# Kernel tuning notes

Measured on AMD Instinct MI355X. Metric: run time of the kernel, lower is better.

Reference implementation:

```python
import jax, jax.numpy as jnp
import numpy as np

HIDDEN = 2048
INPUT = 128
BATCH = 2048


def setup_inputs() -> dict:
    key = jax.random.key(0)
    k = jax.random.split(key, 7)
    inp = {
        "input": jax.random.normal(k[0], (BATCH, INPUT), dtype=jnp.float32),
        "hx_real": jax.random.normal(k[1], (BATCH, HIDDEN), dtype=jnp.float32),
        "hx_imag": jax.random.normal(k[2], (BATCH, HIDDEN), dtype=jnp.float32),
        "W_unitary": jax.random.normal(k[3], (5 * HIDDEN, INPUT), dtype=jnp.float32) / np.sqrt(INPUT),
        "b_unitary": jax.random.normal(k[4], (5 * HIDDEN,), dtype=jnp.float32) * 0.01,
        "beta": jnp.zeros((HIDDEN,), dtype=jnp.float32),
        "permutation": jax.random.permutation(k[5], HIDDEN).astype(jnp.int32),
    }
    return inp


def _householder_apply(v, h):
    # (I - 2 v v^H) h = h - 2 v (v^H h); same math as materializing the matrix.
    proj = jnp.sum(jnp.conj(v) * h, axis=-1, keepdims=True)
    return h - 2.0 * v * proj


def reference(input, hx_real, hx_imag, W_unitary, b_unitary, beta, permutation):
    hx = hx_real + 1j * hx_imag  # (B, H) complex64
    up = input @ W_unitary.T + b_unitary  # (B, 5H)
    phases = jnp.exp(1j * up)  # complex64, unit modulus
    d1, d2, d3, r1, r2 = jnp.split(phases, 5, axis=-1)

    h = jnp.fft.fft(d1 * hx, axis=-1)
    h = _householder_apply(r1, h)
    h = jnp.fft.ifft(d2 * h[:, permutation], axis=-1)
    h = d3 * _householder_apply(r2, h)

    # ModReLU: relu(|z| + beta) * exp(1j * angle(z))
    mag = jnp.abs(h)
    new_mag = jax.nn.relu(mag + beta)
    h = new_mag * jnp.exp(1j * jnp.angle(h))
    return h
```

## Files before the change

kernel.cpp:

```cpp
#include <hip/hip_runtime.h>

#define HID 2048
#define FIVEH 10240
#define INP 128
#define BATCH 2048

typedef _Float16 half8 __attribute__((ext_vector_type(8)));
typedef float f32x4 __attribute__((ext_vector_type(4)));

__global__ __launch_bounds__(256) void convert_f16(const float* __restrict__ src,
                                                   _Float16* __restrict__ dst) {
  int idx = (blockIdx.x * 256 + threadIdx.x) * 8;
  float4 a = *(const float4*)(src + idx);
  float4 b = *(const float4*)(src + idx + 4);
  half8 h;
  h[0] = (_Float16)a.x; h[1] = (_Float16)a.y; h[2] = (_Float16)a.z; h[3] = (_Float16)a.w;
  h[4] = (_Float16)b.x; h[5] = (_Float16)b.y; h[6] = (_Float16)b.z; h[7] = (_Float16)b.w;
  *(half8*)(dst + idx) = h;
}

__global__ __launch_bounds__(256) void gemm_up(const _Float16* __restrict__ Ah,
                                               const _Float16* __restrict__ Wh,
                                               const float* __restrict__ bias,
                                               _Float16* __restrict__ up16,
                                               int row0, int nrows) {
  int tid = threadIdx.x, wave = tid >> 6, lane = tid & 63;
  int mg_count = nrows >> 6;
  int wid = blockIdx.x * 4 + wave;
  if (wid >= mg_count * 80) return;
  int mg = wid % mg_count;
  int ns = wid / mg_count;
  int nl = lane & 15, quad = lane >> 4;

  half8 af[4][4];
#pragma unroll
  for (int mt = 0; mt < 4; ++mt) {
    const _Float16* arow = Ah + (size_t)(row0 + mg * 64 + mt * 16 + nl) * INP + quad * 8;
#pragma unroll
    for (int ks = 0; ks < 4; ++ks) af[mt][ks] = *(const half8*)(arow + ks * 32);
  }

#pragma unroll
  for (int nt = 0; nt < 8; ++nt) {
    int ncol = ns * 128 + nt * 16 + nl;
    const _Float16* wrow = Wh + (size_t)ncol * INP + quad * 8;
    half8 bf[4];
#pragma unroll
    for (int ks = 0; ks < 4; ++ks) bf[ks] = *(const half8*)(wrow + ks * 32);
    float bv = bias[ncol];
#pragma unroll
    for (int mt = 0; mt < 4; ++mt) {
      f32x4 acc = {0.f, 0.f, 0.f, 0.f};
#pragma unroll
      for (int ks = 0; ks < 4; ++ks)
        acc = __builtin_amdgcn_mfma_f32_16x16x32_f16(af[mt][ks], bf[ks], acc, 0, 0, 0);
      int mbase = mg * 64 + mt * 16 + quad * 4;
#pragma unroll
      for (int r = 0; r < 4; ++r)
        up16[(size_t)(mbase + r) * FIVEH + ncol] = (_Float16)(acc[r] + bv);
    }
  }
}

__device__ __forceinline__ void fft_r4(float2*& src, float2*& dst, int tid, float sgn) {
#pragma unroll
  for (int t = 0; t < 4; ++t) {
    int i = tid + (t << 8);
    float2 a = src[i], b = src[i + 1024];
    float4 o;
    o.x = a.x + b.x; o.y = a.y + b.y;
    o.z = a.x - b.x; o.w = a.y - b.y;
    *(float4*)&dst[2 * i] = o;
  }
  __syncthreads();
  { float2* t = src; src = dst; dst = t; }

#pragma unroll
  for (int pass = 0; pass < 5; ++pass) {
    const int L = 2 << (2 * pass);
    const float co = sgn * 1.5707963267948966f / (float)L;
#pragma unroll
    for (int t = 0; t < 2; ++t) {
      int i = tid + (t << 8);
      int k = i & (L - 1);
      int base4 = ((i - k) << 2) + k;
      float2 x0 = src[i], x1 = src[i + 512], x2 = src[i + 1024], x3 = src[i + 1536];
      float ang = co * (float)k;
      float s1, c1; __sincosf(ang, &s1, &c1);
      float c2 = c1 * c1 - s1 * s1, s2 = 2.f * c1 * s1;
      float c3 = c1 * c2 - s1 * s2, s3 = c1 * s2 + s1 * c2;
      float y1r = x1.x * c1 - x1.y * s1, y1i = x1.x * s1 + x1.y * c1;
      float y2r = x2.x * c2 - x2.y * s2, y2i = x2.x * s2 + x2.y * c2;
      float y3r = x3.x * c3 - x3.y * s3, y3i = x3.x * s3 + x3.y * c3;
      float t0r = x0.x + y2r, t0i = x0.y + y2i;
      float t1r = x0.x - y2r, t1i = x0.y - y2i;
      float t2r = y1r + y3r, t2i = y1i + y3i;
      float t3r = y1r - y3r, t3i = y1i - y3i;
      dst[base4]         = make_float2(t0r + t2r, t0i + t2i);
      dst[base4 + 2 * L] = make_float2(t0r - t2r, t0i - t2i);
      dst[base4 + L]     = make_float2(t1r - sgn * t3i, t1i + sgn * t3r);
      dst[base4 + 3 * L] = make_float2(t1r + sgn * t3i, t1i - sgn * t3r);
    }
    __syncthreads();
    { float2* t = src; src = dst; dst = t; }
  }
}

__device__ __forceinline__ void block_reduce2(float& pr, float& pi,
                                              float* redr, float* redi, int tid) {
  for (int off = 32; off > 0; off >>= 1) {
    pr += __shfl_down(pr, off, 64);
    pi += __shfl_down(pi, off, 64);
  }
  if ((tid & 63) == 0) { redr[tid >> 6] = pr; redi[tid >> 6] = pi; }
  __syncthreads();
  pr = redr[0] + redr[1] + redr[2] + redr[3];
  pi = redi[0] + redi[1] + redi[2] + redi[3];
  __syncthreads();
}

#define ROW_PIPELINE(UP)                                                        \
  float2 *ca = sA, *cb = sB;                                                    \
  fft_r4(ca, cb, tid, -1.0f);                                                   \
  float cc[8], ss[8];                                                           \
  {                                                                             \
    float pr = 0.f, pi = 0.f;                                                   \
    _Pragma("unroll") for (int e = 0; e < 8; ++e) {                             \
      int k = tid + (e << 8);                                                   \
      float sv, cv; __sincosf(UP(e, 3), &sv, &cv);                              \
      cc[e] = cv; ss[e] = sv;                                                   \
      float2 h = ca[k];                                                         \
      pr += cv * h.x + sv * h.y;                                                \
      pi += cv * h.y - sv * h.x;                                                \
    }                                                                           \
    block_reduce2(pr, pi, redr, redi, tid);                                     \
    _Pragma("unroll") for (int e = 0; e < 8; ++e) {                             \
      int k = tid + (e << 8);                                                   \
      float2 h = ca[k];                                                         \
      h.x -= 2.f * (cc[e] * pr - ss[e] * pi);                                   \
      h.y -= 2.f * (cc[e] * pi + ss[e] * pr);                                   \
      ca[k] = h;                                                                \
    }                                                                           \
  }                                                                             \
  __syncthreads();                                                              \
  _Pragma("unroll") for (int e = 0; e < 8; ++e) {                               \
    int k = tid + (e << 8);                                                     \
    float sv, cv; __sincosf(UP(e, 1), &sv, &cv);                                \
    float2 h = ca[perm[k]];                                                     \
    cb[k] = make_float2(cv * h.x - sv * h.y, cv * h.y + sv * h.x);              \
  }                                                                             \
  __syncthreads();                                                              \
  { float2* t = ca; ca = cb; cb = t; }                                          \
  fft_r4(ca, cb, tid, 1.0f);                                                    \
  float prj_r, prj_i;                                                           \
  {                                                                             \
    float pr = 0.f, pi = 0.f;                                                   \
    _Pragma("unroll") for (int e = 0; e < 8; ++e) {                             \
      int k = tid + (e << 8);                                                   \
      float sv, cv; __sincosf(UP(e, 4), &sv, &cv);                              \
      cc[e] = cv; ss[e] = sv;                                                   \
      float2 h = ca[k];                                                         \
      pr += cv * h.x + sv * h.y;                                                \
      pi += cv * h.y - sv * h.x;                                                \
    }                                                                           \
    block_reduce2(pr, pi, redr, redi, tid);                                     \
    prj_r = pr; prj_i = pi;                                                     \
  }                                                                             \
  const float invN = 1.0f / (float)HID;                                         \
  _Pragma("unroll") for (int e = 0; e < 8; ++e) {                               \
    int k = tid + (e << 8);                                                     \
    float2 h = ca[k];                                                           \
    float hr = h.x - 2.f * (cc[e] * prj_r - ss[e] * prj_i);                     \
    float hi = h.y - 2.f * (cc[e] * prj_i + ss[e] * prj_r);                     \
    float s3, c3; __sincosf(UP(e, 2), &s3, &c3);                                \
    float zr = (c3 * hr - s3 * hi) * invN;                                      \
    float zi = (c3 * hi + s3 * hr) * invN;                                      \
    float mag = sqrtf(zr * zr + zi * zi);                                       \
    float nm = mag + beta[k];                                                   \
    nm = nm > 0.f ? nm : 0.f;                                                   \
    float orr, oii;                                                             \
    if (mag > 0.f) { float sc = nm / mag; orr = zr * sc; oii = zi * sc; }       \
    else { orr = nm; oii = 0.f; }                                               \
    long m = (long)b * HID + k;                                                 \
    if (omode == 1) {                                                           \
      const long half = (long)BATCH * HID;                                      \
      if (half + m < out_size_l) { out[m] = orr; out[half + m] = oii; }         \
    } else if (omode == 0) {                                                    \
      if (2 * m + 1 < out_size_l) {                                             \
        float2 o; o.x = orr; o.y = oii;                                         \
        *(float2*)(out + 2 * m) = o;                                            \
      }                                                                         \
    } else {                                                                    \
      if (m < out_size_l) out[m] = orr;                                         \
    }                                                                           \
  }

__global__ __launch_bounds__(256) void urnn_row(const _Float16* __restrict__ up16,
                                                const float* __restrict__ hxr,
                                                const float* __restrict__ hxi,
                                                const float* __restrict__ beta,
                                                const int* __restrict__ perm,
                                                float* __restrict__ out,
                                                int row0, long out_size_l, int omode) {
  __shared__ float2 sA[HID], sB[HID];
  __shared__ float redr[4], redi[4];

  int tid = threadIdx.x;
  int b = row0 + blockIdx.x;
  const _Float16* uprow = up16 + (size_t)blockIdx.x * FIVEH;
#define UPG(e, s) ((float)uprow[(s) * HID + tid + ((e) << 8)])

#pragma unroll
  for (int e = 0; e < 8; ++e) {
    int k = tid + (e << 8);
    float sv, cv; __sincosf(UPG(e, 0), &sv, &cv);
    float hr = hxr[(size_t)b * HID + k];
    float hi = hxi[(size_t)b * HID + k];
    sA[k] = make_float2(cv * hr - sv * hi, cv * hi + sv * hr);
  }
  __syncthreads();
  ROW_PIPELINE(UPG)
#undef UPG
}

__global__ __launch_bounds__(256) void urnn_fused(const float* __restrict__ A,
                                                  const float* __restrict__ W,
                                                  const float* __restrict__ bias,
                                                  const float* __restrict__ hxr,
                                                  const float* __restrict__ hxi,
                                                  const float* __restrict__ beta,
                                                  const int* __restrict__ perm,
                                                  float* __restrict__ out,
                                                  long out_size_l, int omode) {
  __shared__ float2 sA[HID], sB[HID];
  __shared__ float redr[4], redi[4];
  __shared__ float4 xs4[INP / 4];

  int tid = threadIdx.x;
  int b = blockIdx.x;

  if (tid < INP / 4) xs4[tid] = ((const float4*)(A + (size_t)b * INP))[tid];
  __syncthreads();

  float upreg[40];
#pragma unroll
  for (int se = 0; se < 40; ++se) {
    int n = ((se >> 3) << 11) + ((se & 7) << 8) + tid;
    upreg[se] = bias[n];
  }
  for (int kb = 0; kb < 4; ++kb) {
    float4 xv[8];
#pragma unroll
    for (int j = 0; j < 8; ++j) xv[j] = xs4[kb * 8 + j];
#pragma unroll
    for (int se = 0; se < 40; ++se) {
      int n = ((se >> 3) << 11) + ((se & 7) << 8) + tid;
      const float4* wr = (const float4*)(W + (size_t)n * INP + (kb << 5));
      float a = 0.f;
#pragma unroll
      for (int j = 0; j < 8; ++j) {
        float4 wv = wr[j];
        a += xv[j].x * wv.x + xv[j].y * wv.y + xv[j].z * wv.z + xv[j].w * wv.w;
      }
      upreg[se] += a;
    }
  }
#define UPR(e, s) (upreg[(s) * 8 + (e)])
#pragma unroll
  for (int e = 0; e < 8; ++e) {
    int k = tid + (e << 8);
    float sv, cv; __sincosf(UPR(e, 0), &sv, &cv);
    float hr = hxr[(size_t)b * HID + k];
    float hi = hxi[(size_t)b * HID + k];
    sA[k] = make_float2(cv * hr - sv * hi, cv * hi + sv * hr);
  }
  __syncthreads();
  ROW_PIPELINE(UPR)
#undef UPR
}

extern "C" void kernel_launch(void* const* d_in, const int* in_sizes, int n_in,
                              void* d_out, int out_size, void* d_ws, size_t ws_size,
                              hipStream_t stream) {
  const float* input   = (const float*)d_in[0];
  const float* hx_real = (const float*)d_in[1];
  const float* hx_imag = (const float*)d_in[2];
  const float* W       = (const float*)d_in[3];
  const float* bvec    = (const float*)d_in[4];
  const float* beta    = (const float*)d_in[5];
  const int*   perm    = (const int*)d_in[6];

  int omode;
  if (out_size == BATCH * HID) omode = 2;
  else if (out_size == 2 * BATCH * HID) omode = 1;
  else omode = 0;

  const size_t na = (size_t)BATCH * INP;
  const size_t nw = (size_t)FIVEH * INP;
  const size_t fixed = (na + nw) * sizeof(_Float16);
  const size_t rowbytes = (size_t)FIVEH * sizeof(_Float16);
  long chunk = (ws_size > fixed) ? (long)((ws_size - fixed) / rowbytes) : 0;
  if (chunk > BATCH) chunk = BATCH;
  chunk &= ~63L;

  if (chunk >= 64) {
    _Float16* Ah = (_Float16*)d_ws;
    _Float16* Wh = Ah + na;
    _Float16* up16 = (_Float16*)((char*)d_ws + fixed);
    convert_f16<<<(int)(na / 2048), 256, 0, stream>>>(input, Ah);
    convert_f16<<<(int)(nw / 2048), 256, 0, stream>>>(W, Wh);
    for (long row0 = 0; row0 < BATCH; row0 += chunk) {
      int rows = (int)((row0 + chunk <= BATCH) ? chunk : (BATCH - row0));
      int waves = (rows >> 6) * 80;
      gemm_up<<<(waves + 3) / 4, 256, 0, stream>>>(Ah, Wh, bvec, up16, (int)row0, rows);
      urnn_row<<<rows, 256, 0, stream>>>(up16, hx_real, hx_imag, beta, perm,
                                         (float*)d_out, (int)row0, (long)out_size, omode);
    }
  } else {
    urnn_fused<<<BATCH, 256, 0, stream>>>(input, W, bvec, hx_real, hx_imag, beta, perm,
                                          (float*)d_out, (long)out_size, omode);
  }
}
```

Measured before the change: 155.1 us.

## Store FFT shared buffers as half2 and fuse fp16 conversion into GEMM

```diff
diff --git a/kernel.cpp b/kernel.cpp
--- a/kernel.cpp
+++ b/kernel.cpp
@@ -1,4 +1,5 @@
 #include <hip/hip_runtime.h>
+#include <hip/hip_fp16.h>
 
 #define HID 2048
 #define FIVEH 10240
@@ -8,19 +9,17 @@
 typedef _Float16 half8 __attribute__((ext_vector_type(8)));
 typedef float f32x4 __attribute__((ext_vector_type(4)));
 
-__global__ __launch_bounds__(256) void convert_f16(const float* __restrict__ src,
-                                                   _Float16* __restrict__ dst) {
-  int idx = (blockIdx.x * 256 + threadIdx.x) * 8;
-  float4 a = *(const float4*)(src + idx);
-  float4 b = *(const float4*)(src + idx + 4);
+__device__ __forceinline__ half8 cvt8(const float* p) {
+  float4 a = *(const float4*)p;
+  float4 b = *(const float4*)(p + 4);
   half8 h;
   h[0] = (_Float16)a.x; h[1] = (_Float16)a.y; h[2] = (_Float16)a.z; h[3] = (_Float16)a.w;
   h[4] = (_Float16)b.x; h[5] = (_Float16)b.y; h[6] = (_Float16)b.z; h[7] = (_Float16)b.w;
-  *(half8*)(dst + idx) = h;
-}
-
-__global__ __launch_bounds__(256) void gemm_up(const _Float16* __restrict__ Ah,
-                                               const _Float16* __restrict__ Wh,
+  return h;
+}
+
+__global__ __launch_bounds__(256) void gemm_up(const float* __restrict__ A,
+                                               const float* __restrict__ W,
                                                const float* __restrict__ bias,
                                                _Float16* __restrict__ up16,
                                                int row0, int nrows) {
@@ -35,18 +34,18 @@
   half8 af[4][4];
 #pragma unroll
   for (int mt = 0; mt < 4; ++mt) {
-    const _Float16* arow = Ah + (size_t)(row0 + mg * 64 + mt * 16 + nl) * INP + quad * 8;
-#pragma unroll
-    for (int ks = 0; ks < 4; ++ks) af[mt][ks] = *(const half8*)(arow + ks * 32);
+    const float* arow = A + (size_t)(row0 + mg * 64 + mt * 16 + nl) * INP + quad * 8;
+#pragma unroll
+    for (int ks = 0; ks < 4; ++ks) af[mt][ks] = cvt8(arow + ks * 32);
   }
 
 #pragma unroll
   for (int nt = 0; nt < 8; ++nt) {
     int ncol = ns * 128 + nt * 16 + nl;
-    const _Float16* wrow = Wh + (size_t)ncol * INP + quad * 8;
+    const float* wrow = W + (size_t)ncol * INP + quad * 8;
     half8 bf[4];
 #pragma unroll
-    for (int ks = 0; ks < 4; ++ks) bf[ks] = *(const half8*)(wrow + ks * 32);
+    for (int ks = 0; ks < 4; ++ks) bf[ks] = cvt8(wrow + ks * 32);
     float bv = bias[ncol];
 #pragma unroll
     for (int mt = 0; mt < 4; ++mt) {
@@ -62,18 +61,23 @@
   }
 }
 
-__device__ __forceinline__ void fft_r4(float2*& src, float2*& dst, int tid, float sgn) {
+__device__ __forceinline__ float2 h2ld(const __half2* p, int i) {
+  return __half22float2(p[i]);
+}
+__device__ __forceinline__ void h2st(__half2* p, int i, float x, float y) {
+  p[i] = __floats2half2_rn(x, y);
+}
+
+__device__ __forceinline__ void fft_r4(__half2*& src, __half2*& dst, int tid, float sgn) {
 #pragma unroll
   for (int t = 0; t < 4; ++t) {
     int i = tid + (t << 8);
-    float2 a = src[i], b = src[i + 1024];
-    float4 o;
-    o.x = a.x + b.x; o.y = a.y + b.y;
-    o.z = a.x - b.x; o.w = a.y - b.y;
-    *(float4*)&dst[2 * i] = o;
-  }
-  __syncthreads();
-  { float2* t = src; src = dst; dst = t; }
+    float2 a = h2ld(src, i), b = h2ld(src, i + 1024);
+    h2st(dst, 2 * i,     a.x + b.x, a.y + b.y);
+    h2st(dst, 2 * i + 1, a.x - b.x, a.y - b.y);
+  }
+  __syncthreads();
+  { __half2* t = src; src = dst; dst = t; }
 
 #pragma unroll
   for (int pass = 0; pass < 5; ++pass) {
@@ -84,7 +88,8 @@
       int i = tid + (t << 8);
       int k = i & (L - 1);
       int base4 = ((i - k) << 2) + k;
-      float2 x0 = src[i], x1 = src[i + 512], x2 = src[i + 1024], x3 = src[i + 1536];
+      float2 x0 = h2ld(src, i),        x1 = h2ld(src, i + 512);
+      float2 x2 = h2ld(src, i + 1024), x3 = h2ld(src, i + 1536);
       float ang = co * (float)k;
       float s1, c1; __sincosf(ang, &s1, &c1);
       float c2 = c1 * c1 - s1 * s1, s2 = 2.f * c1 * s1;
@@ -96,13 +101,13 @@
       float t1r = x0.x - y2r, t1i = x0.y - y2i;
       float t2r = y1r + y3r, t2i = y1i + y3i;
       float t3r = y1r - y3r, t3i = y1i - y3i;
-      dst[base4]         = make_float2(t0r + t2r, t0i + t2i);
-      dst[base4 + 2 * L] = make_float2(t0r - t2r, t0i - t2i);
-      dst[base4 + L]     = make_float2(t1r - sgn * t3i, t1i + sgn * t3r);
-      dst[base4 + 3 * L] = make_float2(t1r + sgn * t3i, t1i - sgn * t3r);
+      h2st(dst, base4,         t0r + t2r, t0i + t2i);
+      h2st(dst, base4 + 2 * L, t0r - t2r, t0i - t2i);
+      h2st(dst, base4 + L,     t1r - sgn * t3i, t1i + sgn * t3r);
+      h2st(dst, base4 + 3 * L, t1r + sgn * t3i, t1i - sgn * t3r);
     }
     __syncthreads();
-    { float2* t = src; src = dst; dst = t; }
+    { __half2* t = src; src = dst; dst = t; }
   }
 }
 
@@ -120,7 +125,7 @@
 }
 
 #define ROW_PIPELINE(UP)                                                        \
-  float2 *ca = sA, *cb = sB;                                                    \
+  __half2 *ca = sA, *cb = sB;                                                   \
   fft_r4(ca, cb, tid, -1.0f);                                                   \
   float cc[8], ss[8];                                                           \
   {                                                                             \
@@ -129,28 +134,28 @@
       int k = tid + (e << 8);                                                   \
       float sv, cv; __sincosf(UP(e, 3), &sv, &cv);                              \
       cc[e] = cv; ss[e] = sv;                                                   \
-      float2 h = ca[k];                                                         \
+      float2 h = h2ld(ca, k);                                                   \
       pr += cv * h.x + sv * h.y;                                                \
       pi += cv * h.y - sv * h.x;                                                \
     }                                                                           \
     block_reduce2(pr, pi, redr, redi, tid);                                     \
     _Pragma("unroll") for (int e = 0; e < 8; ++e) {                             \
       int k = tid + (e << 8);                                                   \
-      float2 h = ca[k];                                                         \
-      h.x -= 2.f * (cc[e] * pr - ss[e] * pi);                                   \
-      h.y -= 2.f * (cc[e] * pi + ss[e] * pr);                                   \
-      ca[k] = h;                                                                \
+      float2 h = h2ld(ca, k);                                                   \
+      h2st(ca, k, h.x - 2.f * (cc[e] * pr - ss[e] * pi),                        \
+                  h.y - 2.f * (cc[e] * pi + ss[e] * pr));                       \
     }                                                                           \
   }                                                                             \
   __syncthreads();                                                              \
+  const float invN = 1.0f / (float)HID;                                         \
   _Pragma("unroll") for (int e = 0; e < 8; ++e) {                               \
     int k = tid + (e << 8);                                                     \
     float sv, cv; __sincosf(UP(e, 1), &sv, &cv);                                \
-    float2 h = ca[perm[k]];                                                     \
-    cb[k] = make_float2(cv * h.x - sv * h.y, cv * h.y + sv * h.x);              \
+    float2 h = h2ld(ca, perm[k]);                                               \
+    h2st(cb, k, (cv * h.x - sv * h.y) * invN, (cv * h.y + sv * h.x) * invN);    \
   }                                                                             \
   __syncthreads();                                                              \
-  { float2* t = ca; ca = cb; cb = t; }                                          \
+  { __half2* t = ca; ca = cb; cb = t; }                                         \
   fft_r4(ca, cb, tid, 1.0f);                                                    \
   float prj_r, prj_i;                                                           \
   {                                                                             \
@@ -159,22 +164,21 @@
       int k = tid + (e << 8);                                                   \
       float sv, cv; __sincosf(UP(e, 4), &sv, &cv);                              \
       cc[e] = cv; ss[e] = sv;                                                   \
-      float2 h = ca[k];                                                         \
+      float2 h = h2ld(ca, k);                                                   \
       pr += cv * h.x + sv * h.y;                                                \
       pi += cv * h.y - sv * h.x;                                                \
     }                                                                           \
     block_reduce2(pr, pi, redr, redi, tid);                                     \
     prj_r = pr; prj_i = pi;                                                     \
   }                                                                             \
-  const float invN = 1.0f / (float)HID;                                         \
   _Pragma("unroll") for (int e = 0; e < 8; ++e) {                               \
     int k = tid + (e << 8);                                                     \
-    float2 h = ca[k];                                                           \
+    float2 h = h2ld(ca, k);                                                     \
     float hr = h.x - 2.f * (cc[e] * prj_r - ss[e] * prj_i);                     \
     float hi = h.y - 2.f * (cc[e] * prj_i + ss[e] * prj_r);                     \
     float s3, c3; __sincosf(UP(e, 2), &s3, &c3);                                \
-    float zr = (c3 * hr - s3 * hi) * invN;                                      \
-    float zi = (c3 * hi + s3 * hr) * invN;                                      \
+    float zr = c3 * hr - s3 * hi;                                               \
+    float zi = c3 * hi + s3 * hr;                                               \
     float mag = sqrtf(zr * zr + zi * zi);                                       \
     float nm = mag + beta[k];                                                   \
     nm = nm > 0.f ? nm : 0.f;                                                   \
@@ -195,14 +199,14 @@
     }                                                                           \
   }
 
-__global__ __launch_bounds__(256) void urnn_row(const _Float16* __restrict__ up16,
-                                                const float* __restrict__ hxr,
-                                                const float* __restrict__ hxi,
-                                                const float* __restrict__ beta,
-                                                const int* __restrict__ perm,
-                                                float* __restrict__ out,
-                                                int row0, long out_size_l, int omode) {
-  __shared__ float2 sA[HID], sB[HID];
+__global__ __launch_bounds__(256, 8) void urnn_row(const _Float16* __restrict__ up16,
+                                                   const float* __restrict__ hxr,
+                                                   const float* __restrict__ hxi,
+                                                   const float* __restrict__ beta,
+                                                   const int* __restrict__ perm,
+                                                   float* __restrict__ out,
+                                                   int row0, long out_size_l, int omode) {
+  __shared__ __half2 sA[HID], sB[HID];
   __shared__ float redr[4], redi[4];
 
   int tid = threadIdx.x;
@@ -216,7 +220,7 @@
     float sv, cv; __sincosf(UPG(e, 0), &sv, &cv);
     float hr = hxr[(size_t)b * HID + k];
     float hi = hxi[(size_t)b * HID + k];
-    sA[k] = make_float2(cv * hr - sv * hi, cv * hi + sv * hr);
+    h2st(sA, k, cv * hr - sv * hi, cv * hi + sv * hr);
   }
   __syncthreads();
   ROW_PIPELINE(UPG)
@@ -232,7 +236,7 @@
                                                   const int* __restrict__ perm,
                                                   float* __restrict__ out,
                                                   long out_size_l, int omode) {
-  __shared__ float2 sA[HID], sB[HID];
+  __shared__ __half2 sA[HID], sB[HID];
   __shared__ float redr[4], redi[4];
   __shared__ float4 xs4[INP / 4];
 
@@ -272,7 +276,7 @@
     float sv, cv; __sincosf(UPR(e, 0), &sv, &cv);
     float hr = hxr[(size_t)b * HID + k];
     float hi = hxi[(size_t)b * HID + k];
-    sA[k] = make_float2(cv * hr - sv * hi, cv * hi + sv * hr);
+    h2st(sA, k, cv * hr - sv * hi, cv * hi + sv * hr);
   }
   __syncthreads();
   ROW_PIPELINE(UPR)
@@ -295,24 +299,17 @@
   else if (out_size == 2 * BATCH * HID) omode = 1;
   else omode = 0;
 
-  const size_t na = (size_t)BATCH * INP;
-  const size_t nw = (size_t)FIVEH * INP;
-  const size_t fixed = (na + nw) * sizeof(_Float16);
   const size_t rowbytes = (size_t)FIVEH * sizeof(_Float16);
-  long chunk = (ws_size > fixed) ? (long)((ws_size - fixed) / rowbytes) : 0;
+  long chunk = (long)(ws_size / rowbytes);
   if (chunk > BATCH) chunk = BATCH;
   chunk &= ~63L;
 
   if (chunk >= 64) {
-    _Float16* Ah = (_Float16*)d_ws;
-    _Float16* Wh = Ah + na;
-    _Float16* up16 = (_Float16*)((char*)d_ws + fixed);
-    convert_f16<<<(int)(na / 2048), 256, 0, stream>>>(input, Ah);
-    convert_f16<<<(int)(nw / 2048), 256, 0, stream>>>(W, Wh);
+    _Float16* up16 = (_Float16*)d_ws;
     for (long row0 = 0; row0 < BATCH; row0 += chunk) {
       int rows = (int)((row0 + chunk <= BATCH) ? chunk : (BATCH - row0));
       int waves = (rows >> 6) * 80;
-      gemm_up<<<(waves + 3) / 4, 256, 0, stream>>>(Ah, Wh, bvec, up16, (int)row0, rows);
+      gemm_up<<<(waves + 3) / 4, 256, 0, stream>>>(input, W, bvec, up16, (int)row0, rows);
       urnn_row<<<rows, 256, 0, stream>>>(up16, hx_real, hx_imag, beta, perm,
                                          (float*)d_out, (int)row0, (long)out_size, omode);
     }
```

New measurement: 168.8 us. 8.9% more time.
